# Kernel optimization log

Hardware: AMD Instinct MI355X
Metric: run time of the kernel (lower is better)

The kernel has to match this reference:

```python
import jax, jax.numpy as jnp
import numpy as np

HIDDEN = 256
NUM_STEPS = 3
N_NODES = 200000
N_GRAPHS = 512


def setup_inputs() -> dict:
    key = jax.random.key(0)
    ks = jax.random.split(key, 8)
    h = HIDDEN
    x = jax.random.normal(ks[0], (N_NODES, h), dtype=jnp.float32)
    batch = jnp.sort(jax.random.randint(ks[1], (N_NODES,), 0, N_GRAPHS)).astype(jnp.int64)
    s_ih = 1.0 / np.sqrt(2 * h)
    s_hh = 1.0 / np.sqrt(h)
    # LSTM (input 2h -> hidden h), PyTorch gate order i,f,g,o
    W_ih = jax.random.uniform(ks[2], (4 * h, 2 * h), jnp.float32, -s_ih, s_ih)
    W_hh = jax.random.uniform(ks[3], (4 * h, h), jnp.float32, -s_hh, s_hh)
    b_ih = jax.random.uniform(ks[4], (4 * h,), jnp.float32, -s_hh, s_hh)
    b_hh = jax.random.uniform(ks[5], (4 * h,), jnp.float32, -s_hh, s_hh)
    # out_proj: Linear(2h -> h)
    s_o = 1.0 / np.sqrt(2 * h)
    W_out = jax.random.uniform(ks[6], (h, 2 * h), jnp.float32, -s_o, s_o)
    b_out = jax.random.uniform(ks[7], (h,), jnp.float32, -s_o, s_o)
    return {"x": x, "batch": batch, "W_ih": W_ih, "W_hh": W_hh,
            "b_ih": b_ih, "b_hh": b_hh, "W_out": W_out, "b_out": b_out,
            "n_graphs": N_GRAPHS}


def _set2set(x, batch, W_ih, W_hh, b_ih, b_hh, n_graphs):
    h = x.shape[1]
    hs = jnp.zeros((n_graphs, h), x.dtype)
    cs = jnp.zeros((n_graphs, h), x.dtype)
    q_star = jnp.zeros((n_graphs, 2 * h), x.dtype)
    for _ in range(NUM_STEPS):
        # LSTM step (PyTorch gate order: i, f, g, o)
        gates = q_star @ W_ih.T + hs @ W_hh.T + (b_ih + b_hh)  # [B, 4h]
        i_g, f_g, g_g, o_g = jnp.split(gates, 4, axis=-1)
        cs = jax.nn.sigmoid(f_g) * cs + jax.nn.sigmoid(i_g) * jnp.tanh(g_g)
        hs = jax.nn.sigmoid(o_g) * jnp.tanh(cs)
        q = hs  # [B, h]
        # attention logits per node
        e = jnp.sum(x * q[batch], axis=-1)  # [N]
        # segment softmax over nodes of each graph
        m = jax.ops.segment_max(e, batch, num_segments=n_graphs)
        a = jnp.exp(e - m[batch])
        denom = jax.ops.segment_sum(a, batch, num_segments=n_graphs)
        a = a / denom[batch]
        # weighted readout
        r = jax.ops.segment_sum(a[:, None] * x, batch, num_segments=n_graphs)  # [B, h]
        q_star = jnp.concatenate([q, r], axis=-1)  # [B, 2h]
    return q_star


def reference(x, batch, W_ih, W_hh, b_ih, b_hh, W_out, b_out, n_graphs):
    q_star = _set2set(x, batch.astype(jnp.int32), W_ih, W_hh, b_ih, b_hh, n_graphs)
    return q_star @ W_out.T + b_out
```

## Files before the change

kernel.cpp:

```cpp
#include <hip/hip_runtime.h>

#define HID 256
#define NG 512

__device__ __forceinline__ float sigmoidf_(float v) { return 1.f / (1.f + __expf(-v)); }

__global__ __launch_bounds__(256) void setup_kernel(
    const float* __restrict__ W_ih, const float* __restrict__ W_hh,
    const float* __restrict__ b_ih, const float* __restrict__ b_hh,
    float* __restrict__ Wcat, float* __restrict__ bcat,
    const int* __restrict__ batch, int n, int* __restrict__ starts)
{
    int b = blockIdx.x;
    if (b < 2048) {
        int idx = b * 256 + threadIdx.x;
        int k = idx & 511;
        float v = W_ih[idx];
        if (k < 256) v += W_hh[(idx >> 9) * 256 + k];
        Wcat[idx] = v;
        if (idx < 1024) bcat[idx] = b_ih[idx] + b_hh[idx];
    } else {
        int g = (b - 2048) * 256 + threadIdx.x;
        if (g > NG) return;
        if (g == NG) { starts[NG] = n; return; }
        int lo = 0, hi = n;
        while (lo < hi) {
            int mid = (lo + hi) >> 1;
            if (batch[mid] < g) lo = mid + 1; else hi = mid;
        }
        starts[g] = lo;
    }
}

__global__ __launch_bounds__(512, 4) void attn_kernel(
    const float* __restrict__ x, const int* __restrict__ starts,
    const float* __restrict__ gates_p,
    const float* __restrict__ bcat, float* __restrict__ cs,
    float* __restrict__ qs, int step0)
{
    __shared__ __align__(16) float ql[HID];
    __shared__ __align__(16) float red[8][HID];
    __shared__ float mw[8], lw[8];

    const int g = blockIdx.x;
    const int tid = threadIdx.x;

    if (tid < 256) {
        float ig, fg, gg, og, cp;
        if (step0) {
            ig = bcat[tid]; fg = bcat[256 + tid]; gg = bcat[512 + tid]; og = bcat[768 + tid];
            cp = 0.f;
        } else {
            ig = bcat[tid]; fg = bcat[256 + tid]; gg = bcat[512 + tid]; og = bcat[768 + tid];
            const float* a = gates_p + (size_t)g * 1024;
            const size_t ss = (size_t)512 * 1024;
            #pragma unroll
            for (int z = 0; z < 4; ++z) {
                const float* az = a + z * ss;
                ig += az[tid]; fg += az[256 + tid]; gg += az[512 + tid]; og += az[768 + tid];
            }
            cp = cs[g * HID + tid];
        }
        float cn = sigmoidf_(fg) * cp + sigmoidf_(ig) * tanhf(gg);
        float h  = sigmoidf_(og) * tanhf(cn);
        cs[g * HID + tid] = cn;
        qs[(size_t)g * 512 + tid] = h;
        ql[tid] = h;
    }
    __syncthreads();

    const int s0 = starts[g];
    const int nn = starts[g + 1] - s0;
    if (nn <= 0) {
        if (tid < 256) qs[(size_t)g * 512 + HID + tid] = 0.f;
        return;
    }

    const int w = tid >> 6, lane = tid & 63;
    const int j = lane >> 3;
    const int s = lane & 7;

    const float4* qp = (const float4*)&ql[s * 4];

    const int nch = (nn + 7) >> 3;
    const int last = s0 + nn - 1;
    const float NEG = -3.402823466e38f;

    float m_run = NEG, l_run = 0.f;
    float4 racc[8] = {};
    float4 xc[8], xn[8];

    int c = w;
    if (c < nch) {
        int node = s0 + c * 8 + j; if (node > last) node = last;
        const float* bp = x + (size_t)node * HID + s * 4;
        #pragma unroll
        for (int k = 0; k < 8; ++k) xc[k] = *(const float4*)(bp + k * 32);
    }
    for (; c < nch; c += 8) {
        if (c + 8 < nch) {
            int node = s0 + (c + 8) * 8 + j; if (node > last) node = last;
            const float* bp = x + (size_t)node * HID + s * 4;
            #pragma unroll
            for (int k = 0; k < 8; ++k) xn[k] = *(const float4*)(bp + k * 32);
        }
        const bool valid = (c * 8 + j) < nn;

        float e = 0.f;
        #pragma unroll
        for (int k = 0; k < 8; ++k) {
            float4 q = qp[k * 8];
            e += xc[k].x * q.x + xc[k].y * q.y + xc[k].z * q.z + xc[k].w * q.w;
        }
        e += __shfl_xor(e, 1); e += __shfl_xor(e, 2); e += __shfl_xor(e, 4);
        e = valid ? e : NEG;

        float mc = e;
        mc = fmaxf(mc, __shfl_xor(mc, 8));
        mc = fmaxf(mc, __shfl_xor(mc, 16));
        mc = fmaxf(mc, __shfl_xor(mc, 32));
        float m_new = fmaxf(m_run, mc);
        float alpha = __expf(m_run - m_new);
        float p = valid ? __expf(e - m_new) : 0.f;
        float ps = p;
        ps += __shfl_xor(ps, 8); ps += __shfl_xor(ps, 16); ps += __shfl_xor(ps, 32);
        l_run = l_run * alpha + ps;
        m_run = m_new;
        #pragma unroll
        for (int k = 0; k < 8; ++k) {
            racc[k].x = racc[k].x * alpha + p * xc[k].x;
            racc[k].y = racc[k].y * alpha + p * xc[k].y;
            racc[k].z = racc[k].z * alpha + p * xc[k].z;
            racc[k].w = racc[k].w * alpha + p * xc[k].w;
        }
        #pragma unroll
        for (int k = 0; k < 8; ++k) xc[k] = xn[k];
    }

    #pragma unroll
    for (int k = 0; k < 8; ++k) {
        racc[k].x += __shfl_xor(racc[k].x, 8);
        racc[k].y += __shfl_xor(racc[k].y, 8);
        racc[k].z += __shfl_xor(racc[k].z, 8);
        racc[k].w += __shfl_xor(racc[k].w, 8);
        racc[k].x += __shfl_xor(racc[k].x, 16);
        racc[k].y += __shfl_xor(racc[k].y, 16);
        racc[k].z += __shfl_xor(racc[k].z, 16);
        racc[k].w += __shfl_xor(racc[k].w, 16);
        racc[k].x += __shfl_xor(racc[k].x, 32);
        racc[k].y += __shfl_xor(racc[k].y, 32);
        racc[k].z += __shfl_xor(racc[k].z, 32);
        racc[k].w += __shfl_xor(racc[k].w, 32);
    }
    if (j == 0) {
        #pragma unroll
        for (int k = 0; k < 8; ++k) *(float4*)&red[w][k * 32 + s * 4] = racc[k];
        if (s == 0) { mw[w] = m_run; lw[w] = l_run; }
    }
    __syncthreads();

    if (tid < 256) {
        float M = NEG;
        #pragma unroll
        for (int v = 0; v < 8; ++v) M = fmaxf(M, mw[v]);
        float L = 0.f, r = 0.f;
        #pragma unroll
        for (int v = 0; v < 8; ++v) {
            float f = __expf(mw[v] - M);
            L += lw[v] * f;
            r += red[v][tid] * f;
        }
        qs[(size_t)g * 512 + HID + tid] = r / L;
    }
}

__global__ __launch_bounds__(256) void gemm_splitk(
    const float* __restrict__ A, int lda,
    const float* __restrict__ B, int ldb,
    float* __restrict__ Cp, int ldc, int KS, size_t slice_stride)
{
    __shared__ float As[16][76];
    __shared__ float Bs[16][76];
    const int tid = threadIdx.x;
    const int tx = tid & 15, ty = tid >> 4;
    const int m0 = blockIdx.y * 64, n0 = blockIdx.x * 64;
    const int kb = blockIdx.z * KS;
    const int r = tid >> 2, kc = (tid & 3) << 2;
    float acc[4][4] = {};

    const float* Ap = &A[(size_t)(m0 + r) * lda + kb + kc];
    const float* Bp = &B[(size_t)(n0 + r) * ldb + kb + kc];
    float4 av = *(const float4*)Ap;
    float4 bv = *(const float4*)Bp;

    for (int k0 = 0; k0 < KS; k0 += 16) {
        As[kc + 0][r] = av.x; As[kc + 1][r] = av.y; As[kc + 2][r] = av.z; As[kc + 3][r] = av.w;
        Bs[kc + 0][r] = bv.x; Bs[kc + 1][r] = bv.y; Bs[kc + 2][r] = bv.z; Bs[kc + 3][r] = bv.w;
        __syncthreads();
        if (k0 + 16 < KS) {
            av = *(const float4*)(Ap + k0 + 16);
            bv = *(const float4*)(Bp + k0 + 16);
        }
        #pragma unroll
        for (int kk = 0; kk < 16; ++kk) {
            float4 a = *(const float4*)&As[kk][ty << 2];
            float4 b = *(const float4*)&Bs[kk][tx << 2];
            acc[0][0] += a.x * b.x; acc[0][1] += a.x * b.y; acc[0][2] += a.x * b.z; acc[0][3] += a.x * b.w;
            acc[1][0] += a.y * b.x; acc[1][1] += a.y * b.y; acc[1][2] += a.y * b.z; acc[1][3] += a.y * b.w;
            acc[2][0] += a.z * b.x; acc[2][1] += a.z * b.y; acc[2][2] += a.z * b.z; acc[2][3] += a.z * b.w;
            acc[3][0] += a.w * b.x; acc[3][1] += a.w * b.y; acc[3][2] += a.w * b.z; acc[3][3] += a.w * b.w;
        }
        __syncthreads();
    }
    float* out = Cp + blockIdx.z * slice_stride;
    #pragma unroll
    for (int i = 0; i < 4; ++i) {
        float4 o = make_float4(acc[i][0], acc[i][1], acc[i][2], acc[i][3]);
        *(float4*)&out[(size_t)(m0 + ty * 4 + i) * ldc + n0 + (tx << 2)] = o;
    }
}

__global__ __launch_bounds__(256) void finalize_out(
    const float* __restrict__ op, const float* __restrict__ b_out,
    float* __restrict__ out)
{
    int i = blockIdx.x * 256 + threadIdx.x;
    if (i < 512 * 256) {
        float v = op[i] + op[131072 + i] + op[262144 + i] + op[393216 + i] + b_out[i & 255];
        out[i] = v;
    }
}

extern "C" void kernel_launch(void* const* d_in, const int* in_sizes, int n_in,
                              void* d_out, int out_size, void* d_ws, size_t ws_size,
                              hipStream_t stream)
{
    const float* x     = (const float*)d_in[0];
    const int*   batch = (const int*)d_in[1];
    const float* W_ih  = (const float*)d_in[2];
    const float* W_hh  = (const float*)d_in[3];
    const float* b_ih  = (const float*)d_in[4];
    const float* b_hh  = (const float*)d_in[5];
    const float* W_out = (const float*)d_in[6];
    const float* b_out = (const float*)d_in[7];
    float* out = (float*)d_out;
    const int n = in_sizes[1];
    (void)n_in; (void)out_size; (void)ws_size;

    char* ws = (char*)d_ws;
    float* qs      = (float*)(ws);
    float* cs      = (float*)(ws + 0x100000);
    float* gates_p = (float*)(ws + 0x180000);
    float* Wcat    = (float*)(ws + 0x980000);
    float* bcat    = (float*)(ws + 0xB80000);
    int*   starts  = (int*)  (ws + 0xB81000);
    float* out_p   = (float*)(ws + 0xB90000);

    setup_kernel<<<2051, 256, 0, stream>>>(W_ih, W_hh, b_ih, b_hh, Wcat, bcat,
                                           batch, n, starts);

    for (int step = 0; step < 3; ++step) {
        if (step > 0) {
            gemm_splitk<<<dim3(16, 8, 4), 256, 0, stream>>>(
                qs, 512, Wcat, 512, gates_p, 1024, 128, (size_t)512 * 1024);
        }
        attn_kernel<<<NG, 512, 0, stream>>>(
            x, starts, gates_p, bcat, cs, qs, step == 0);
    }
    gemm_splitk<<<dim3(4, 8, 4), 256, 0, stream>>>(
        qs, 512, W_out, 512, out_p, 256, 128, (size_t)512 * 256);
    finalize_out<<<512, 256, 0, stream>>>(out_p, b_out, out);
}
```

Baseline: 491.2 us.

## Shrink attention blocks to 4 waves with triple-buffered x loads and register-held query

The attention kernel now runs with 256 threads (4 waves) per graph instead of 512, and each wave walks its chunks with a three-deep rotating register buffer (P/Q/R) so two chunk loads are in flight while one is computed. The query vector is held in registers rather than re-read from LDS every chunk, and the final cross-wave merge is unrolled over 4 partials. The aim is to keep more memory requests outstanding per wave and cut LDS traffic during the streaming pass over x. The cost is higher register pressure (three 8-float4 buffers plus accumulators and query), which may lower occupancy, and halving the waves per graph lowers the parallelism available for each graph.

```diff
diff --git a/kernel.cpp b/kernel.cpp
--- a/kernel.cpp
+++ b/kernel.cpp
@@ -32,26 +32,60 @@
     }
 }
 
-__global__ __launch_bounds__(512, 4) void attn_kernel(
+
+#define LOADB(BUF, CIDX) do {                                               \
+    int node_ = s0 + (CIDX) * 8 + j; if (node_ > last) node_ = last;        \
+    const float* bp_ = x + (size_t)node_ * HID + s * 4;                     \
+    _Pragma("unroll")                                                       \
+    for (int k = 0; k < 8; ++k) BUF[k] = *(const float4*)(bp_ + k * 32);    \
+} while (0)
+
+#define COMPUTE(BUF, CIDX) do {                                             \
+    const bool valid_ = ((CIDX) * 8 + j) < nn;                              \
+    float e_ = 0.f;                                                         \
+    _Pragma("unroll")                                                       \
+    for (int k = 0; k < 8; ++k)                                             \
+        e_ += BUF[k].x * qf[k].x + BUF[k].y * qf[k].y                       \
+            + BUF[k].z * qf[k].z + BUF[k].w * qf[k].w;                      \
+    e_ += __shfl_xor(e_, 1); e_ += __shfl_xor(e_, 2); e_ += __shfl_xor(e_, 4); \
+    e_ = valid_ ? e_ : NEG;                                                 \
+    float mc_ = e_;                                                         \
+    mc_ = fmaxf(mc_, __shfl_xor(mc_, 8));                                   \
+    mc_ = fmaxf(mc_, __shfl_xor(mc_, 16));                                  \
+    mc_ = fmaxf(mc_, __shfl_xor(mc_, 32));                                  \
+    float mnew_ = fmaxf(m_run, mc_);                                        \
+    float alpha_ = __expf(m_run - mnew_);                                   \
+    float p_ = valid_ ? __expf(e_ - mnew_) : 0.f;                           \
+    float ps_ = p_;                                                         \
+    ps_ += __shfl_xor(ps_, 8); ps_ += __shfl_xor(ps_, 16); ps_ += __shfl_xor(ps_, 32); \
+    l_run = l_run * alpha_ + ps_;                                           \
+    m_run = mnew_;                                                          \
+    _Pragma("unroll")                                                       \
+    for (int k = 0; k < 8; ++k) {                                           \
+        racc[k].x = racc[k].x * alpha_ + p_ * BUF[k].x;                     \
+        racc[k].y = racc[k].y * alpha_ + p_ * BUF[k].y;                     \
+        racc[k].z = racc[k].z * alpha_ + p_ * BUF[k].z;                     \
+        racc[k].w = racc[k].w * alpha_ + p_ * BUF[k].w;                     \
+    }                                                                       \
+} while (0)
+
+__global__ __launch_bounds__(256) void attn_kernel(
     const float* __restrict__ x, const int* __restrict__ starts,
     const float* __restrict__ gates_p,
     const float* __restrict__ bcat, float* __restrict__ cs,
     float* __restrict__ qs, int step0)
 {
     __shared__ __align__(16) float ql[HID];
-    __shared__ __align__(16) float red[8][HID];
-    __shared__ float mw[8], lw[8];
+    __shared__ __align__(16) float red[4][HID];
+    __shared__ float mw[4], lw[4];
 
     const int g = blockIdx.x;
     const int tid = threadIdx.x;
 
-    if (tid < 256) {
-        float ig, fg, gg, og, cp;
-        if (step0) {
-            ig = bcat[tid]; fg = bcat[256 + tid]; gg = bcat[512 + tid]; og = bcat[768 + tid];
-            cp = 0.f;
-        } else {
-            ig = bcat[tid]; fg = bcat[256 + tid]; gg = bcat[512 + tid]; og = bcat[768 + tid];
+    {
+        float ig = bcat[tid], fg = bcat[256 + tid], gg = bcat[512 + tid], og = bcat[768 + tid];
+        float cp = 0.f;
+        if (!step0) {
             const float* a = gates_p + (size_t)g * 1024;
             const size_t ss = (size_t)512 * 1024;
             #pragma unroll
@@ -67,20 +101,19 @@
         qs[(size_t)g * 512 + tid] = h;
         ql[tid] = h;
     }
-    __syncthreads();
 
     const int s0 = starts[g];
     const int nn = starts[g + 1] - s0;
-    if (nn <= 0) {
-        if (tid < 256) qs[(size_t)g * 512 + HID + tid] = 0.f;
-        return;
-    }
+    if (nn <= 0) { qs[(size_t)g * 512 + HID + tid] = 0.f; return; }
+    __syncthreads();
 
     const int w = tid >> 6, lane = tid & 63;
     const int j = lane >> 3;
     const int s = lane & 7;
 
-    const float4* qp = (const float4*)&ql[s * 4];
+    float4 qf[8];
+    #pragma unroll
+    for (int k = 0; k < 8; ++k) qf[k] = *(const float4*)&ql[k * 32 + s * 4];
 
     const int nch = (nn + 7) >> 3;
     const int last = s0 + nn - 1;
@@ -88,53 +121,20 @@
 
     float m_run = NEG, l_run = 0.f;
     float4 racc[8] = {};
-    float4 xc[8], xn[8];
+    float4 P[8], Q[8], R[8];
 
     int c = w;
-    if (c < nch) {
-        int node = s0 + c * 8 + j; if (node > last) node = last;
-        const float* bp = x + (size_t)node * HID + s * 4;
-        #pragma unroll
-        for (int k = 0; k < 8; ++k) xc[k] = *(const float4*)(bp + k * 32);
-    }
-    for (; c < nch; c += 8) {
-        if (c + 8 < nch) {
-            int node = s0 + (c + 8) * 8 + j; if (node > last) node = last;
-            const float* bp = x + (size_t)node * HID + s * 4;
-            #pragma unroll
-            for (int k = 0; k < 8; ++k) xn[k] = *(const float4*)(bp + k * 32);
-        }
-        const bool valid = (c * 8 + j) < nn;
-
-        float e = 0.f;
-        #pragma unroll
-        for (int k = 0; k < 8; ++k) {
-            float4 q = qp[k * 8];
-            e += xc[k].x * q.x + xc[k].y * q.y + xc[k].z * q.z + xc[k].w * q.w;
-        }
-        e += __shfl_xor(e, 1); e += __shfl_xor(e, 2); e += __shfl_xor(e, 4);
-        e = valid ? e : NEG;
-
-        float mc = e;
-        mc = fmaxf(mc, __shfl_xor(mc, 8));
-        mc = fmaxf(mc, __shfl_xor(mc, 16));
-        mc = fmaxf(mc, __shfl_xor(mc, 32));
-        float m_new = fmaxf(m_run, mc);
-        float alpha = __expf(m_run - m_new);
-        float p = valid ? __expf(e - m_new) : 0.f;
-        float ps = p;
-        ps += __shfl_xor(ps, 8); ps += __shfl_xor(ps, 16); ps += __shfl_xor(ps, 32);
-        l_run = l_run * alpha + ps;
-        m_run = m_new;
-        #pragma unroll
-        for (int k = 0; k < 8; ++k) {
-            racc[k].x = racc[k].x * alpha + p * xc[k].x;
-            racc[k].y = racc[k].y * alpha + p * xc[k].y;
-            racc[k].z = racc[k].z * alpha + p * xc[k].z;
-            racc[k].w = racc[k].w * alpha + p * xc[k].w;
-        }
-        #pragma unroll
-        for (int k = 0; k < 8; ++k) xc[k] = xn[k];
+    if (c < nch)     LOADB(P, c);
+    if (c + 4 < nch) LOADB(Q, c + 4);
+    for (; c < nch; c += 12) {
+        if (c + 8 < nch)  LOADB(R, c + 8);
+        COMPUTE(P, c);
+        if (c + 4 >= nch) break;
+        if (c + 12 < nch) LOADB(P, c + 12);
+        COMPUTE(Q, c + 4);
+        if (c + 8 >= nch) break;
+        if (c + 16 < nch) LOADB(Q, c + 16);
+        COMPUTE(R, c + 8);
     }
 
     #pragma unroll
@@ -159,19 +159,12 @@
     }
     __syncthreads();
 
-    if (tid < 256) {
-        float M = NEG;
-        #pragma unroll
-        for (int v = 0; v < 8; ++v) M = fmaxf(M, mw[v]);
-        float L = 0.f, r = 0.f;
-        #pragma unroll
-        for (int v = 0; v < 8; ++v) {
-            float f = __expf(mw[v] - M);
-            L += lw[v] * f;
-            r += red[v][tid] * f;
-        }
-        qs[(size_t)g * 512 + HID + tid] = r / L;
-    }
+    float M = fmaxf(fmaxf(mw[0], mw[1]), fmaxf(mw[2], mw[3]));
+    float f0 = __expf(mw[0] - M), f1 = __expf(mw[1] - M);
+    float f2 = __expf(mw[2] - M), f3 = __expf(mw[3] - M);
+    float L = lw[0] * f0 + lw[1] * f1 + lw[2] * f2 + lw[3] * f3;
+    float r = red[0][tid] * f0 + red[1][tid] * f1 + red[2][tid] * f2 + red[3][tid] * f3;
+    qs[(size_t)g * 512 + HID + tid] = r / L;
 }
 
 __global__ __launch_bounds__(256) void gemm_splitk(
@@ -264,7 +257,7 @@
             gemm_splitk<<<dim3(16, 8, 4), 256, 0, stream>>>(
                 qs, 512, Wcat, 512, gates_p, 1024, 128, (size_t)512 * 1024);
         }
-        attn_kernel<<<NG, 512, 0, stream>>>(
+        attn_kernel<<<NG, 256, 0, stream>>>(
             x, starts, gates_p, bcat, cs, qs, step == 0);
     }
     gemm_splitk<<<dim3(4, 8, 4), 256, 0, stream>>>(
```

After: 412.1 us. 1.19x faster.

## Split per-graph attention across four blocks with separate merge kernel

Applied to the files above, without the earlier changes.

Each graph's node range is now handled by four 256-thread blocks instead of one 512-thread block. The partial max, sum and readout from each block go to a workspace buffer, and a new merge kernel combines them. The cell state is double-buffered so that redundant blocks can recompute the LSTM gates without racing. The online softmax now rescales its running values only when the maximum increases, and the gate GEMM uses a 2-way K split instead of 4-way. The aim is better CU occupancy and load balance for the memory-bound pass over x. The cost is an extra kernel launch per step and the LSTM cell being recomputed four times per graph.

```diff
diff --git a/kernel.cpp b/kernel.cpp
--- a/kernel.cpp
+++ b/kernel.cpp
@@ -32,56 +32,51 @@
     }
 }
 
-__global__ __launch_bounds__(512, 4) void attn_kernel(
+__global__ __launch_bounds__(256, 4) void attn_kernel(
     const float* __restrict__ x, const int* __restrict__ starts,
     const float* __restrict__ gates_p,
-    const float* __restrict__ bcat, float* __restrict__ cs,
-    float* __restrict__ qs, int step0)
+    const float* __restrict__ bcat,
+    const float* __restrict__ cs_r, float* __restrict__ cs_w,
+    float* __restrict__ qs, float* __restrict__ pr, int step0)
 {
     __shared__ __align__(16) float ql[HID];
-    __shared__ __align__(16) float red[8][HID];
-    __shared__ float mw[8], lw[8];
-
-    const int g = blockIdx.x;
+    __shared__ __align__(16) float red[4][HID];
+    __shared__ float mw[4], lw[4];
+
+    const int g = blockIdx.x >> 2, part = blockIdx.x & 3;
     const int tid = threadIdx.x;
 
-    if (tid < 256) {
-        float ig, fg, gg, og, cp;
-        if (step0) {
-            ig = bcat[tid]; fg = bcat[256 + tid]; gg = bcat[512 + tid]; og = bcat[768 + tid];
-            cp = 0.f;
-        } else {
-            ig = bcat[tid]; fg = bcat[256 + tid]; gg = bcat[512 + tid]; og = bcat[768 + tid];
+    {
+        float ig = bcat[tid], fg = bcat[256 + tid], gg = bcat[512 + tid], og = bcat[768 + tid];
+        float cp = 0.f;
+        if (!step0) {
             const float* a = gates_p + (size_t)g * 1024;
             const size_t ss = (size_t)512 * 1024;
             #pragma unroll
-            for (int z = 0; z < 4; ++z) {
+            for (int z = 0; z < 2; ++z) {
                 const float* az = a + z * ss;
                 ig += az[tid]; fg += az[256 + tid]; gg += az[512 + tid]; og += az[768 + tid];
             }
-            cp = cs[g * HID + tid];
+            cp = cs_r[g * HID + tid];
         }
         float cn = sigmoidf_(fg) * cp + sigmoidf_(ig) * tanhf(gg);
         float h  = sigmoidf_(og) * tanhf(cn);
-        cs[g * HID + tid] = cn;
-        qs[(size_t)g * 512 + tid] = h;
+        if (part == 0) {
+            cs_w[g * HID + tid] = cn;
+            qs[(size_t)g * 512 + tid] = h;
+        }
         ql[tid] = h;
     }
-    __syncthreads();
 
     const int s0 = starts[g];
     const int nn = starts[g + 1] - s0;
-    if (nn <= 0) {
-        if (tid < 256) qs[(size_t)g * 512 + HID + tid] = 0.f;
-        return;
-    }
+    if (nn <= 0) return;
+    __syncthreads();
 
     const int w = tid >> 6, lane = tid & 63;
     const int j = lane >> 3;
     const int s = lane & 7;
 
-    const float4* qp = (const float4*)&ql[s * 4];
-
     const int nch = (nn + 7) >> 3;
     const int last = s0 + nn - 1;
     const float NEG = -3.402823466e38f;
@@ -90,16 +85,16 @@
     float4 racc[8] = {};
     float4 xc[8], xn[8];
 
-    int c = w;
+    int c = part * 4 + w;
     if (c < nch) {
         int node = s0 + c * 8 + j; if (node > last) node = last;
         const float* bp = x + (size_t)node * HID + s * 4;
         #pragma unroll
         for (int k = 0; k < 8; ++k) xc[k] = *(const float4*)(bp + k * 32);
     }
-    for (; c < nch; c += 8) {
-        if (c + 8 < nch) {
-            int node = s0 + (c + 8) * 8 + j; if (node > last) node = last;
+    for (; c < nch; c += 16) {
+        if (c + 16 < nch) {
+            int node = s0 + (c + 16) * 8 + j; if (node > last) node = last;
             const float* bp = x + (size_t)node * HID + s * 4;
             #pragma unroll
             for (int k = 0; k < 8; ++k) xn[k] = *(const float4*)(bp + k * 32);
@@ -109,29 +104,35 @@
         float e = 0.f;
         #pragma unroll
         for (int k = 0; k < 8; ++k) {
-            float4 q = qp[k * 8];
+            float4 q = *(const float4*)&ql[k * 32 + s * 4];
             e += xc[k].x * q.x + xc[k].y * q.y + xc[k].z * q.z + xc[k].w * q.w;
         }
         e += __shfl_xor(e, 1); e += __shfl_xor(e, 2); e += __shfl_xor(e, 4);
         e = valid ? e : NEG;
 
-        float mc = e;
-        mc = fmaxf(mc, __shfl_xor(mc, 8));
+        float mc = fmaxf(e, __shfl_xor(e, 8));
         mc = fmaxf(mc, __shfl_xor(mc, 16));
         mc = fmaxf(mc, __shfl_xor(mc, 32));
-        float m_new = fmaxf(m_run, mc);
-        float alpha = __expf(m_run - m_new);
-        float p = valid ? __expf(e - m_new) : 0.f;
+        if (mc > m_run) {
+            float alpha = __expf(m_run - mc);
+            l_run *= alpha;
+            #pragma unroll
+            for (int k = 0; k < 8; ++k) {
+                racc[k].x *= alpha; racc[k].y *= alpha;
+                racc[k].z *= alpha; racc[k].w *= alpha;
+            }
+            m_run = mc;
+        }
+        float p = valid ? __expf(e - m_run) : 0.f;
         float ps = p;
         ps += __shfl_xor(ps, 8); ps += __shfl_xor(ps, 16); ps += __shfl_xor(ps, 32);
-        l_run = l_run * alpha + ps;
-        m_run = m_new;
+        l_run += ps;
         #pragma unroll
         for (int k = 0; k < 8; ++k) {
-            racc[k].x = racc[k].x * alpha + p * xc[k].x;
-            racc[k].y = racc[k].y * alpha + p * xc[k].y;
-            racc[k].z = racc[k].z * alpha + p * xc[k].z;
-            racc[k].w = racc[k].w * alpha + p * xc[k].w;
+            racc[k].x += p * xc[k].x;
+            racc[k].y += p * xc[k].y;
+            racc[k].z += p * xc[k].z;
+            racc[k].w += p * xc[k].w;
         }
         #pragma unroll
         for (int k = 0; k < 8; ++k) xc[k] = xn[k];
@@ -159,19 +160,31 @@
     }
     __syncthreads();
 
-    if (tid < 256) {
-        float M = NEG;
-        #pragma unroll
-        for (int v = 0; v < 8; ++v) M = fmaxf(M, mw[v]);
-        float L = 0.f, r = 0.f;
-        #pragma unroll
-        for (int v = 0; v < 8; ++v) {
-            float f = __expf(mw[v] - M);
-            L += lw[v] * f;
-            r += red[v][tid] * f;
-        }
-        qs[(size_t)g * 512 + HID + tid] = r / L;
-    }
+    float M = fmaxf(fmaxf(mw[0], mw[1]), fmaxf(mw[2], mw[3]));
+    float f0 = __expf(mw[0] - M), f1 = __expf(mw[1] - M);
+    float f2 = __expf(mw[2] - M), f3 = __expf(mw[3] - M);
+    float L = lw[0] * f0 + lw[1] * f1 + lw[2] * f2 + lw[3] * f3;
+    float R = red[0][tid] * f0 + red[1][tid] * f1 + red[2][tid] * f2 + red[3][tid] * f3;
+    float* pb = pr + (size_t)(((size_t)g << 2) + part) * 260;
+    pb[tid] = R;
+    if (tid == 0) { pb[256] = M; pb[257] = L; }
+}
+
+__global__ __launch_bounds__(256) void merge_kernel(
+    const float* __restrict__ pr, const int* __restrict__ starts,
+    float* __restrict__ qs)
+{
+    const int g = blockIdx.x, tid = threadIdx.x;
+    const int nn = starts[g + 1] - starts[g];
+    if (nn <= 0) { qs[(size_t)g * 512 + HID + tid] = 0.f; return; }
+    const float* pb = pr + (size_t)g * 4 * 260;
+    float m0 = pb[256], m1 = pb[260 + 256], m2 = pb[2 * 260 + 256], m3 = pb[3 * 260 + 256];
+    float M = fmaxf(fmaxf(m0, m1), fmaxf(m2, m3));
+    float f0 = __expf(m0 - M), f1 = __expf(m1 - M);
+    float f2 = __expf(m2 - M), f3 = __expf(m3 - M);
+    float L = pb[257] * f0 + pb[260 + 257] * f1 + pb[2 * 260 + 257] * f2 + pb[3 * 260 + 257] * f3;
+    float R = pb[tid] * f0 + pb[260 + tid] * f1 + pb[2 * 260 + tid] * f2 + pb[3 * 260 + tid] * f3;
+    qs[(size_t)g * 512 + HID + tid] = R / L;
 }
 
 __global__ __launch_bounds__(256) void gemm_splitk(
@@ -249,23 +262,28 @@
 
     char* ws = (char*)d_ws;
     float* qs      = (float*)(ws);
-    float* cs      = (float*)(ws + 0x100000);
-    float* gates_p = (float*)(ws + 0x180000);
-    float* Wcat    = (float*)(ws + 0x980000);
-    float* bcat    = (float*)(ws + 0xB80000);
-    int*   starts  = (int*)  (ws + 0xB81000);
-    float* out_p   = (float*)(ws + 0xB90000);
+    float* csA     = (float*)(ws + 0x100000);
+    float* csB     = (float*)(ws + 0x180000);
+    float* gates_p = (float*)(ws + 0x200000);
+    float* Wcat    = (float*)(ws + 0x600000);
+    float* bcat    = (float*)(ws + 0x800000);
+    int*   starts  = (int*)  (ws + 0x801000);
+    float* pr      = (float*)(ws + 0x810000);
+    float* out_p   = (float*)(ws + 0xA20000);
 
     setup_kernel<<<2051, 256, 0, stream>>>(W_ih, W_hh, b_ih, b_hh, Wcat, bcat,
                                            batch, n, starts);
 
     for (int step = 0; step < 3; ++step) {
         if (step > 0) {
-            gemm_splitk<<<dim3(16, 8, 4), 256, 0, stream>>>(
-                qs, 512, Wcat, 512, gates_p, 1024, 128, (size_t)512 * 1024);
-        }
-        attn_kernel<<<NG, 512, 0, stream>>>(
-            x, starts, gates_p, bcat, cs, qs, step == 0);
+            gemm_splitk<<<dim3(16, 8, 2), 256, 0, stream>>>(
+                qs, 512, Wcat, 512, gates_p, 1024, 256, (size_t)512 * 1024);
+        }
+        const float* cs_r = (step == 2) ? csB : csA;
+        float*       cs_w = (step == 1) ? csB : csA;
+        attn_kernel<<<NG * 4, 256, 0, stream>>>(
+            x, starts, gates_p, bcat, cs_r, cs_w, qs, pr, step == 0);
+        merge_kernel<<<NG, 256, 0, stream>>>(pr, starts, qs);
     }
     gemm_splitk<<<dim3(4, 8, 4), 256, 0, stream>>>(
         qs, 512, W_out, 512, out_p, 256, 128, (size_t)512 * 256);
```

Measured after the change: 530.3 us. 1.08x slower.
